# Optimization experiments

Measured on AMD Instinct MI355X. Metric: run time of the kernel, lower is better.

## Reference

```python
import jax, jax.numpy as jnp
import numpy as np

N = 100000   # nodes per node type (individuals and each attribute type)
D = 128      # embedding_size
A = 3        # number of attribute types
P = 50000    # population size
E = 500000   # edges per individual<->attribute edge type
EF = 500000  # family edges


def _seg_mean(msgs, idx, n):
    # PyG 'mean' aggregation: sum / count, empty segments -> 0
    s = jax.ops.segment_sum(msgs, idx, num_segments=n)
    c = jax.ops.segment_sum(jnp.ones((msgs.shape[0],), msgs.dtype), idx, num_segments=n)
    return s / jnp.maximum(c, 1.0)[:, None]


def setup_inputs() -> dict:
    key = jax.random.key(0)
    ks = jax.random.split(key, 20)
    s = 0.05
    return {
        'x_individuals': jax.random.normal(ks[0], (N, D), jnp.float32),
        'x_attributes': jax.random.normal(ks[1], (A, N, D), jnp.float32),
        'positional_features': jax.random.normal(ks[2], (P, A, D), jnp.float32),
        'population': jax.random.permutation(ks[3], N)[:P],  # unique ids (torch indexed assignment with dup ids is UB)
        'edge_index_attr': jax.random.randint(ks[4], (A, 2, E), 0, N),
        'edge_index_family': jax.random.randint(ks[5], (2, EF), 0, N),
        'proj': jax.random.normal(ks[6], (A, D, D), jnp.float32),  # torch.randn(D,D) per attribute
        'agg_W': jax.random.normal(ks[7], (D, 2 * D), jnp.float32) * s,
        'agg_b': jax.random.normal(ks[8], (D,), jnp.float32) * s,
        'W_l1': jax.random.normal(ks[9], (A, D, D), jnp.float32) * s,
        'b_l1': jax.random.normal(ks[10], (A, D), jnp.float32) * s,
        'W_r1': jax.random.normal(ks[11], (A, D, D), jnp.float32) * s,
        'W_l2': jax.random.normal(ks[12], (A, D, D), jnp.float32) * s,
        'b_l2': jax.random.normal(ks[13], (A, D), jnp.float32) * s,
        'W_r2': jax.random.normal(ks[14], (A, D, D), jnp.float32) * s,
        'W_l3': jax.random.normal(ks[15], (D, D), jnp.float32) * s,
        'b_l3': jax.random.normal(ks[16], (D,), jnp.float32) * s,
        'W_r3': jax.random.normal(ks[17], (D, D), jnp.float32) * s,
    }


def reference(x_individuals, x_attributes, positional_features, proj, agg_W, agg_b,
              W_l1, b_l1, W_r1, W_l2, b_l2, W_r2, W_l3, b_l3, W_r3,
              population, edge_index_attr, edge_index_family):
    relu = jax.nn.relu
    src = edge_index_attr[:, 0, :]  # [A,E] individual side
    dst = edge_index_attr[:, 1, :]  # [A,E] attribute side

    # --- stage 0: apply_edges_on_attributes ---
    esf = jnp.einsum('pai,aio->apo', positional_features, proj)          # [A,P,D]
    cat = jnp.concatenate([x_attributes[:, population, :], esf], -1)     # [A,P,2D]
    h = relu(jnp.einsum('api,oi->apo', cat, agg_W) + agg_b)              # Linear(2D->D) + ReLU
    x_att = x_attributes.at[:, population, :].set(h)

    # --- stage 1: SAGEConv individuals -> attributes (source_to_target) ---
    msgs = x_individuals[src]                                            # [A,E,D]
    agg1 = jax.vmap(lambda m, i: _seg_mean(m, i, N))(msgs, dst)          # [A,N,D]
    x_att = (jnp.einsum('ani,aoi->ano', agg1, W_l1) + b_l1[:, None, :]
             + jnp.einsum('ani,aoi->ano', x_att, W_r1))

    # --- stage 2a: apply_edges_on_individuals (per-attribute inverse projection) ---
    M = jnp.linalg.inv(proj) + jnp.eye(D, dtype=proj.dtype)              # [A,D,D]
    upd = relu(jnp.einsum('api,aio->apo', x_att[:, population, :], M))
    x_att = x_att.at[:, population, :].set(upd)

    # --- stage 2b: SAGEConv with flow target_to_source: messages = attribute feats
    # gathered at edge dst, scatter-mean to edge src (individual ids); root term uses x[1]=x_att ---
    msgs2 = jax.vmap(lambda x, i: x[i])(x_att, dst)                      # [A,E,D]
    agg2 = jax.vmap(lambda m, i: _seg_mean(m, i, N))(msgs2, src)         # [A,N,D]
    x_att_out = (jnp.einsum('ani,aoi->ano', agg2, W_l2) + b_l2[:, None, :]
                 + jnp.einsum('ani,aoi->ano', x_att, W_r2))              # stored under attribute keys (PyG HeteroConv dst-keying)

    # --- stage 3: family SAGEConv (target_to_source) on individuals; x_dict['individuals'] was never
    # overwritten by the earlier HeteroConvs (their outputs were keyed by attribute types) ---
    agg3 = _seg_mean(x_individuals[edge_index_family[1]], edge_index_family[0], N)
    x_ind_out = agg3 @ W_l3.T + b_l3 + x_individuals @ W_r3.T

    return x_ind_out, x_att_out
```

## Files before the change

kernel.cpp:

```cpp
#include <hip/hip_runtime.h>
#include <cstddef>

constexpr int Nn  = 100000;
constexpr int Dd  = 128;
constexpr int Aa  = 3;
constexpr int Pp  = 50000;
constexpr int Ee  = 500000;
constexpr int EFf = 500000;
constexpr int REG = Nn + 1;
constexpr int NCSR = 7;
constexpr int T7  = NCSR * REG;
constexpr int RCH = 8;

__global__ void k_invpop(const int* __restrict__ pop, int* __restrict__ invpop){
  int p = blockIdx.x*256 + threadIdx.x;
  if(p < Pp) invpop[pop[p]] = p;
}

__global__ void k_count(const int* __restrict__ eia, const int* __restrict__ fam,
                        int* __restrict__ cnt){
  int tid = blockIdx.x*256 + threadIdx.x;
  if(tid >= NCSR*Ee) return;
  int c = tid / Ee, e = tid - c*Ee;
  const int* key;
  if(c < 3)       key = eia + (c*2+1)*Ee;
  else if(c < 6)  key = eia + ((c-3)*2)*Ee;
  else            key = fam;
  atomicAdd(&cnt[c*REG + key[e]], 1);
}

__global__ void k_fill(const int* __restrict__ eia, const int* __restrict__ fam,
                       int* __restrict__ cursor, int* __restrict__ ebuf){
  int tid = blockIdx.x*256 + threadIdx.x;
  if(tid >= NCSR*Ee) return;
  int c = tid / Ee, e = tid - c*Ee;
  const int *key, *val;
  if(c < 3){      key = eia + (c*2+1)*Ee;      val = eia + (c*2)*Ee; }
  else if(c < 6){ key = eia + ((c-3)*2)*Ee;    val = eia + ((c-3)*2+1)*Ee; }
  else {          key = fam;                   val = fam + EFf; }
  int pos = atomicAdd(&cursor[c*REG + key[e]], 1);
  ebuf[pos] = val[e];
}

__global__ void k_scan_p1(const int* __restrict__ cnt, int* __restrict__ part){
  int b = blockIdx.x;
  int base = b*1024 + threadIdx.x*4;
  int s = 0;
  #pragma unroll
  for(int j=0;j<4;j++){ int idx=base+j; if(idx<T7) s += cnt[idx]; }
  __shared__ int red[256];
  red[threadIdx.x]=s; __syncthreads();
  for(int off=128; off>0; off>>=1){
    if(threadIdx.x<off) red[threadIdx.x]+=red[threadIdx.x+off];
    __syncthreads();
  }
  if(threadIdx.x==0) part[b]=red[0];
}

__global__ void k_scan_p2(int* __restrict__ part, int nchunks){
  __shared__ int buf[256];
  int t = threadIdx.x;
  int carry = 0;
  for(int base=0; base<nchunks; base+=256){
    int i = base+t;
    int v = (i<nchunks)? part[i] : 0;
    buf[t]=v; __syncthreads();
    for(int off=1; off<256; off<<=1){
      int add = (t>=off)? buf[t-off] : 0;
      __syncthreads();
      buf[t]+=add; __syncthreads();
    }
    if(i<nchunks) part[i] = carry + buf[t] - v;
    carry += buf[255];
    __syncthreads();
  }
}

__global__ void k_scan_p3(const int* __restrict__ cnt, const int* __restrict__ part,
                          int* __restrict__ offs, int* __restrict__ cursor){
  int b = blockIdx.x;
  int t = threadIdx.x;
  int idx0 = b*1024 + t*4;
  int v[4]; int s=0;
  #pragma unroll
  for(int j=0;j<4;j++){ int idx=idx0+j; v[j] = (idx<T7)? cnt[idx] : 0; s += v[j]; }
  __shared__ int buf[256];
  buf[t]=s; __syncthreads();
  for(int off=1; off<256; off<<=1){
    int add = (t>=off)? buf[t-off] : 0;
    __syncthreads();
    buf[t]+=add; __syncthreads();
  }
  int excl = buf[t] - s + part[b];
  #pragma unroll
  for(int j=0;j<4;j++){
    int idx=idx0+j;
    if(idx<T7){ offs[idx]=excl; cursor[idx]=excl; }
    excl += v[j];
  }
}

__global__ __launch_bounds__(1024)
void k_gjn(const float* __restrict__ proj, float* __restrict__ Mf32){
  __shared__ float W[128*256];
  __shared__ float pv[128];
  __shared__ float cand_av[2];
  __shared__ float cand_sv[2];
  __shared__ int   cand_ix[2];

  const int a = blockIdx.x;
  const int t = threadIdx.x;
  const int lane = t & 63, wid = t >> 6;
  const float* A = proj + (size_t)a*Dd*Dd;

  for(int idx=t; idx<128*256; idx+=1024){
    int i = idx>>8, c = idx&255;
    float v = (c<128) ? A[(size_t)i*128+c] : ((c-128==i)?1.f:0.f);
    W[idx]=v;
  }
  __syncthreads();

  for(int k=0;k<128;k++){
    if(t < 128){
      float sv = W[t*256+k];
      float av = (t>=k)? fabsf(sv) : -1.f;
      int ix = t;
      #pragma unroll
      for(int off=32; off; off>>=1){
        float oav = __shfl_xor(av, off);
        float osv = __shfl_xor(sv, off);
        int   oix = __shfl_xor(ix, off);
        if(oav > av){ av=oav; sv=osv; ix=oix; }
      }
      if(lane==0){ cand_av[wid]=av; cand_sv[wid]=sv; cand_ix[wid]=ix; }
    }
    __syncthreads();
    const int   pr     = (cand_av[0] >= cand_av[1]) ? cand_ix[0] : cand_ix[1];
    const float pivinv = 1.f / ((cand_av[0] >= cand_av[1]) ? cand_sv[0] : cand_sv[1]);
    if(t < 256){
      int c = t;
      float vk = W[k*256+c];
      float vp = W[pr*256+c];
      W[k*256+c] = ((c==k)?1.f:vp)*pivinv;
      if(pr!=k) W[pr*256+c] = vk;
    }
    __syncthreads();
    if(t < 128) pv[t] = W[t*256+k];
    __syncthreads();
    {
      int c = t&255, g = t>>8;
      float wk = W[k*256+c];
      #pragma unroll
      for(int m=0;m<32;m++){
        int ll = g + m*4;
        if(ll==k) continue;
        float base = (c==k)? 0.f : W[ll*256+c];
        W[ll*256+c] = fmaf(-pv[ll], wk, base);
      }
    }
    __syncthreads();
  }

  for(int idx=t; idx<128*128; idx+=1024){
    int i = idx>>7, c = idx&127;
    W[i*256+c] = A[idx];
  }
  __syncthreads();
  const int i  = t>>3;
  const int j0 = (t&7)*16;
  double acc[16];
  #pragma unroll
  for(int q=0;q<16;q++) acc[q] = (i==j0+q)? 1.0 : 0.0;
  for(int k=0;k<128;k++){
    double aik = (double)W[i*256+k];
    #pragma unroll
    for(int q=0;q<16;q++)
      acc[q] -= aik * (double)W[k*256+128+j0+q];
  }
  __syncthreads();
  #pragma unroll
  for(int q=0;q<16;q++) W[i*256+j0+q] = (float)acc[q];
  __syncthreads();
  #pragma unroll
  for(int q=0;q<16;q++) acc[q] = (double)W[i*256+128+j0+q];
  for(int k=0;k<128;k++){
    double xik = (double)W[i*256+128+k];
    #pragma unroll
    for(int q=0;q<16;q++)
      acc[q] += xik * (double)W[k*256+j0+q];
  }
  float* Mo = Mf32 + (size_t)a*Dd*Dd + (size_t)i*128 + j0;
  #pragma unroll
  for(int q=0;q<16;q++)
    Mo[q] = (float)(acc[q] + ((i==j0+q)? 1.0 : 0.0));
}

template<int MODE>
__launch_bounds__(256)
__global__ void k_gemm(const float* p1, const float* p2, const float* p3,
                       const float* __restrict__ w1p, const float* __restrict__ w2p,
                       const float* __restrict__ biasp,
                       const int* __restrict__ pop, const int* __restrict__ invpop,
                       float* out, int BPA)
{
  constexpr bool NEEDX2 = (MODE==1 || MODE==2 || MODE==4 || MODE==5);
  const int RPA = (MODE==0||MODE==1||MODE==3) ? Pp : Nn;
  const int a    = (MODE==5) ? 0 : (blockIdx.x / BPA);
  const int bidx = (MODE==5) ? blockIdx.x : (blockIdx.x - a*BPA);

  const int t = threadIdx.x;
  const int wave = t >> 6;
  const int lane = t & 63;
  const int o  = wave*32 + (lane>>1);
  const int ih = lane & 1;

  float4 w1v[16]; float4 w2v[16];
  if constexpr(MODE==0 || MODE==3){
    const float* W = w1p + (size_t)a*Dd*Dd;
    #pragma unroll
    for(int jj=0;jj<16;jj++){
      int i0 = ih*64 + jj*4;
      float4 v;
      v.x = W[(size_t)(i0+0)*Dd + o];
      v.y = W[(size_t)(i0+1)*Dd + o];
      v.z = W[(size_t)(i0+2)*Dd + o];
      v.w = W[(size_t)(i0+3)*Dd + o];
      w1v[jj]=v;
    }
  } else if constexpr(MODE==1){
    const float* b1 = w1p + (size_t)o*256 + ih*64;
    const float* b2 = b1 + 128;
    #pragma unroll
    for(int jj=0;jj<16;jj++){
      w1v[jj] = reinterpret_cast<const float4*>(b1)[jj];
      w2v[jj] = reinterpret_cast<const float4*>(b2)[jj];
    }
  } else {
    const size_t ao = (MODE==5)? (size_t)0 : (size_t)a*Dd*Dd;
    const float* W1 = w1p + ao + (size_t)o*Dd + ih*64;
    const float* W2 = w2p + ao + (size_t)o*Dd + ih*64;
    #pragma unroll
    for(int jj=0;jj<16;jj++){
      w1v[jj] = reinterpret_cast<const float4*>(W1)[jj];
      w2v[jj] = reinterpret_cast<const float4*>(W2)[jj];
    }
  }
  float bval = 0.f;
  if constexpr(MODE==1 || MODE==5) bval = biasp[o];
  else if constexpr(MODE==2 || MODE==4) bval = biasp[a*Dd + o];

  __shared__ float xs1[RCH][Dd];
  __shared__ float xs2[NEEDX2 ? RCH : 1][Dd];

  const int chunks = (RPA + RCH - 1)/RCH;
  for(int ch = bidx; ch < chunks; ch += BPA){
    const int r0 = ch*RCH;
    const int nr = min(RCH, RPA - r0);
    {
      int r = t >> 5;
      int q = t & 31;
      if(r < nr){
        int row = r0 + r;
        const float* s1 = nullptr; const float* s2 = nullptr;
        if constexpr(MODE==0){ s1 = p1 + ((size_t)row*Aa + a)*Dd; }
        else if constexpr(MODE==1){
          s1 = p1 + ((size_t)a*Nn + pop[row])*Dd;
          s2 = p3 + ((size_t)a*Pp + row)*Dd;
        }
        else if constexpr(MODE==2){
          s1 = p1 + ((size_t)a*Nn + row)*Dd;
          int ip = invpop[row];
          s2 = (ip>=0) ? (p2 + ((size_t)a*Pp + ip)*Dd)
                       : (p3 + ((size_t)a*Nn + row)*Dd);
        }
        else if constexpr(MODE==3){ s1 = p1 + ((size_t)a*Nn + pop[row])*Dd; }
        else if constexpr(MODE==4){
          s1 = p1 + ((size_t)a*Nn + row)*Dd;
          s2 = p3 + ((size_t)a*Nn + row)*Dd;
        }
        else { s1 = p1 + (size_t)row*Dd; s2 = p3 + (size_t)row*Dd; }
        reinterpret_cast<float4*>(xs1[r])[q] = reinterpret_cast<const float4*>(s1)[q];
        if constexpr(NEEDX2)
          reinterpret_cast<float4*>(xs2[r])[q] = reinterpret_cast<const float4*>(s2)[q];
      }
    }
    __syncthreads();
    for(int r=0;r<nr;r++){
      float acc = 0.f;
      const float4* x1 = reinterpret_cast<const float4*>(xs1[r]) + ih*16;
      #pragma unroll
      for(int jj=0;jj<16;jj++){
        float4 xv = x1[jj]; float4 wv = w1v[jj];
        acc = fmaf(xv.x,wv.x,acc); acc = fmaf(xv.y,wv.y,acc);
        acc = fmaf(xv.z,wv.z,acc); acc = fmaf(xv.w,wv.w,acc);
      }
      if constexpr(NEEDX2){
        const float4* x2 = reinterpret_cast<const float4*>(xs2[r]) + ih*16;
        #pragma unroll
        for(int jj=0;jj<16;jj++){
          float4 xv = x2[jj]; float4 wv = w2v[jj];
          acc = fmaf(xv.x,wv.x,acc); acc = fmaf(xv.y,wv.y,acc);
          acc = fmaf(xv.z,wv.z,acc); acc = fmaf(xv.w,wv.w,acc);
        }
      }
      acc += __shfl_xor(acc, 1, 64);
      if(ih==0){
        float vout = acc;
        if constexpr(MODE==1 || MODE==2 || MODE==4 || MODE==5) vout += bval;
        if constexpr(MODE==1 || MODE==3) vout = fmaxf(vout, 0.f);
        int row = r0 + r;
        size_t orow;
        if constexpr(MODE==0)      orow = (size_t)a*Pp + row;
        else if constexpr(MODE==1) orow = (size_t)a*Pp + row;
        else if constexpr(MODE==2) orow = (size_t)a*Nn + row;
        else if constexpr(MODE==3) orow = (size_t)a*Nn + pop[row];
        else if constexpr(MODE==4) orow = (size_t)a*Nn + row;
        else                       orow = (size_t)row;
        out[orow*Dd + o] = vout;
      }
    }
    __syncthreads();
  }
}

template<int WHICH>
__global__ void k_seg(const float* __restrict__ src, const int* __restrict__ offs,
                      const int* __restrict__ ebuf, float* __restrict__ dst)
{
  const int nw = gridDim.x * 4;
  int gw = (blockIdx.x*256 + threadIdx.x) >> 6;
  const int lane = threadIdx.x & 63;
  const int ROWS = (WHICH==2) ? Nn : Aa*Nn;
  const int cbase = (WHICH==0)?0 : (WHICH==1)?3 : 6;
  for(int row = gw; row < ROWS; row += nw){
    int aa = (WHICH==2)? 0   : row / Nn;
    int n  = (WHICH==2)? row : row - aa*Nn;
    const int* op = offs + (size_t)(cbase+aa)*REG + n;
    int s = op[0], e = op[1];
    float a0=0.f, a1=0.f;
    for(int j=s;j<e;++j){
      int v = ebuf[j];
      const float* rp = src + ((WHICH==1)? ((size_t)aa*Nn+v) : (size_t)v)*Dd;
      a0 += rp[lane]; a1 += rp[lane+64];
    }
    float sc = (e>s)? 1.f/(float)(e-s) : 0.f;
    float* dp = dst + ((WHICH==2)? (size_t)n : ((size_t)aa*Nn+n))*Dd;
    dp[lane]      = a0*sc;
    dp[lane+64]   = a1*sc;
  }
}

extern "C" void kernel_launch(void* const* d_in, const int* in_sizes, int n_in,
                              void* d_out, int out_size, void* d_ws, size_t ws_size,
                              hipStream_t stream)
{
  const float* xind  = (const float*)d_in[0];
  const float* xattr = (const float*)d_in[1];
  const float* posf  = (const float*)d_in[2];
  const int*   pop   = (const int*)  d_in[3];
  const int*   eia   = (const int*)  d_in[4];
  const int*   fam   = (const int*)  d_in[5];
  const float* proj  = (const float*)d_in[6];
  const float* aggW  = (const float*)d_in[7];
  const float* aggb  = (const float*)d_in[8];
  const float* Wl1   = (const float*)d_in[9];
  const float* bl1   = (const float*)d_in[10];
  const float* Wr1   = (const float*)d_in[11];
  const float* Wl2   = (const float*)d_in[12];
  const float* bl2   = (const float*)d_in[13];
  const float* Wr2   = (const float*)d_in[14];
  const float* Wl3   = (const float*)d_in[15];
  const float* bl3   = (const float*)d_in[16];
  const float* Wr3   = (const float*)d_in[17];

  float* outind = (float*)d_out;
  float* outatt = outind + (size_t)Nn*Dd;

  float* h_buf   = (float*)d_ws;
  float* esf_buf = h_buf   + (size_t)Aa*Pp*Dd;
  float* xatt2   = esf_buf + (size_t)Aa*Pp*Dd;
  int*   ebuf    = (int*)(xatt2 + (size_t)Aa*Nn*Dd);
  int*   cnt     = ebuf   + (size_t)NCSR*Ee;
  int*   offs    = cnt    + 700008;
  int*   cursor  = offs   + 700008;
  int*   part    = cursor + 700008;
  int*   invpop  = part   + 1024;
  float* Mf32    = (float*)(invpop + Nn);

  hipMemsetAsync(cnt,    0,    sizeof(int)*700008, stream);
  hipMemsetAsync(invpop, 0xFF, sizeof(int)*Nn,     stream);

  k_invpop<<<(Pp+255)/256, 256, 0, stream>>>(pop, invpop);
  const int egrid = (NCSR*Ee + 255)/256;
  k_count<<<egrid, 256, 0, stream>>>(eia, fam, cnt);
  const int nchunks = (T7 + 1023)/1024;
  k_scan_p1<<<nchunks, 256, 0, stream>>>(cnt, part);
  k_scan_p2<<<1, 256, 0, stream>>>(part, nchunks);
  k_scan_p3<<<nchunks, 256, 0, stream>>>(cnt, part, offs, cursor);
  k_fill<<<egrid, 256, 0, stream>>>(eia, fam, cursor, ebuf);

  k_gjn<<<Aa, 1024, 0, stream>>>(proj, Mf32);

  const int BPA = 240;
  k_gemm<0><<<Aa*BPA, 256, 0, stream>>>(posf, nullptr, nullptr,
                                        proj, nullptr, nullptr,
                                        pop, invpop, esf_buf, BPA);
  k_gemm<1><<<Aa*BPA, 256, 0, stream>>>(xattr, nullptr, esf_buf,
                                        aggW, nullptr, aggb,
                                        pop, invpop, h_buf, BPA);
  k_seg<0><<<1024, 256, 0, stream>>>(xind, offs, ebuf, outatt);
  k_gemm<2><<<Aa*BPA, 256, 0, stream>>>(outatt, h_buf, xattr,
                                        Wl1, Wr1, bl1,
                                        pop, invpop, xatt2, BPA);
  k_gemm<3><<<Aa*BPA, 256, 0, stream>>>(xatt2, nullptr, nullptr,
                                        Mf32, nullptr, nullptr,
                                        pop, invpop, xatt2, BPA);
  k_seg<1><<<1024, 256, 0, stream>>>(xatt2, offs, ebuf, outatt);
  k_gemm<4><<<Aa*BPA, 256, 0, stream>>>(outatt, nullptr, xatt2,
                                        Wl2, Wr2, bl2,
                                        pop, invpop, outatt, BPA);
  k_seg<2><<<1024, 256, 0, stream>>>(xind, offs, ebuf, outind);
  k_gemm<5><<<Aa*BPA, 256, 0, stream>>>(outind, nullptr, xind,
                                        Wl3, Wr3, bl3,
                                        pop, invpop, outind, Aa*BPA);
}
```

Baseline: 3.849 ms.

## Double-buffer row staging in GEMM kernel with register prefetch and larger grids

The row-tile GEMM kernel now loads the next chunk's input rows into registers while the current chunk is computed from shared memory. Shared tiles are double-buffered, which removes the trailing barrier per chunk. Separately, blocks per attribute for the GEMMs rise from 240 to 960 and the segment-mean grids from 1024 to 2048 blocks, to hide more memory latency. The cost is more shared memory and registers per block, plus more blocks each reloading their weight rows.

```diff
diff --git a/kernel.cpp b/kernel.cpp
--- a/kernel.cpp
+++ b/kernel.cpp
@@ -249,45 +249,54 @@
   if constexpr(MODE==1 || MODE==5) bval = biasp[o];
   else if constexpr(MODE==2 || MODE==4) bval = biasp[a*Dd + o];
 
-  __shared__ float xs1[RCH][Dd];
-  __shared__ float xs2[NEEDX2 ? RCH : 1][Dd];
+  __shared__ float xs1[2][RCH][Dd];
+  __shared__ float xs2[2][NEEDX2 ? RCH : 1][Dd];
 
   const int chunks = (RPA + RCH - 1)/RCH;
+  const int r = t >> 5;
+  const int q = t & 31;
+
+  float4 pre1 = {0,0,0,0}, pre2 = {0,0,0,0};
+  auto prefetch = [&](int chp){
+    if(chp >= chunks) return;
+    if(r >= RPA - chp*RCH) return;
+    int row = chp*RCH + r;
+    const float* s1 = nullptr; const float* s2 = nullptr;
+    if constexpr(MODE==0){ s1 = p1 + ((size_t)row*Aa + a)*Dd; }
+    else if constexpr(MODE==1){
+      s1 = p1 + ((size_t)a*Nn + pop[row])*Dd;
+      s2 = p3 + ((size_t)a*Pp + row)*Dd;
+    }
+    else if constexpr(MODE==2){
+      s1 = p1 + ((size_t)a*Nn + row)*Dd;
+      int ip = invpop[row];
+      s2 = (ip>=0) ? (p2 + ((size_t)a*Pp + ip)*Dd)
+                   : (p3 + ((size_t)a*Nn + row)*Dd);
+    }
+    else if constexpr(MODE==3){ s1 = p1 + ((size_t)a*Nn + pop[row])*Dd; }
+    else if constexpr(MODE==4){
+      s1 = p1 + ((size_t)a*Nn + row)*Dd;
+      s2 = p3 + ((size_t)a*Nn + row)*Dd;
+    }
+    else { s1 = p1 + (size_t)row*Dd; s2 = p3 + (size_t)row*Dd; }
+    pre1 = reinterpret_cast<const float4*>(s1)[q];
+    if constexpr(NEEDX2) pre2 = reinterpret_cast<const float4*>(s2)[q];
+  };
+
+  prefetch(bidx);
+  int buf = 0;
   for(int ch = bidx; ch < chunks; ch += BPA){
-    const int r0 = ch*RCH;
-    const int nr = min(RCH, RPA - r0);
-    {
-      int r = t >> 5;
-      int q = t & 31;
-      if(r < nr){
-        int row = r0 + r;
-        const float* s1 = nullptr; const float* s2 = nullptr;
-        if constexpr(MODE==0){ s1 = p1 + ((size_t)row*Aa + a)*Dd; }
-        else if constexpr(MODE==1){
-          s1 = p1 + ((size_t)a*Nn + pop[row])*Dd;
-          s2 = p3 + ((size_t)a*Pp + row)*Dd;
-        }
-        else if constexpr(MODE==2){
-          s1 = p1 + ((size_t)a*Nn + row)*Dd;
-          int ip = invpop[row];
-          s2 = (ip>=0) ? (p2 + ((size_t)a*Pp + ip)*Dd)
-                       : (p3 + ((size_t)a*Nn + row)*Dd);
-        }
-        else if constexpr(MODE==3){ s1 = p1 + ((size_t)a*Nn + pop[row])*Dd; }
-        else if constexpr(MODE==4){
-          s1 = p1 + ((size_t)a*Nn + row)*Dd;
-          s2 = p3 + ((size_t)a*Nn + row)*Dd;
-        }
-        else { s1 = p1 + (size_t)row*Dd; s2 = p3 + (size_t)row*Dd; }
-        reinterpret_cast<float4*>(xs1[r])[q] = reinterpret_cast<const float4*>(s1)[q];
-        if constexpr(NEEDX2)
-          reinterpret_cast<float4*>(xs2[r])[q] = reinterpret_cast<const float4*>(s2)[q];
-      }
-    }
-    __syncthreads();
-    for(int r=0;r<nr;r++){
+    const int nr = min(RCH, RPA - ch*RCH);
+    if(r < nr){
+      reinterpret_cast<float4*>(xs1[buf][r])[q] = pre1;
+      if constexpr(NEEDX2)
+        reinterpret_cast<float4*>(xs2[buf][r])[q] = pre2;
+    }
+    __syncthreads();
+    prefetch(ch + BPA);
+    for(int rr=0; rr<nr; rr++){
       float acc = 0.f;
-      const float4* x1 = reinterpret_cast<const float4*>(xs1[r]) + ih*16;
+      const float4* x1 = reinterpret_cast<const float4*>(xs1[buf][rr]) + ih*16;
       #pragma unroll
       for(int jj=0;jj<16;jj++){
         float4 xv = x1[jj]; float4 wv = w1v[jj];
@@ -295,7 +304,7 @@
         acc = fmaf(xv.z,wv.z,acc); acc = fmaf(xv.w,wv.w,acc);
       }
       if constexpr(NEEDX2){
-        const float4* x2 = reinterpret_cast<const float4*>(xs2[r]) + ih*16;
+        const float4* x2 = reinterpret_cast<const float4*>(xs2[buf][rr]) + ih*16;
         #pragma unroll
         for(int jj=0;jj<16;jj++){
           float4 xv = x2[jj]; float4 wv = w2v[jj];
@@ -308,7 +317,7 @@
         float vout = acc;
         if constexpr(MODE==1 || MODE==2 || MODE==4 || MODE==5) vout += bval;
         if constexpr(MODE==1 || MODE==3) vout = fmaxf(vout, 0.f);
-        int row = r0 + r;
+        int row = ch*RCH + rr;
         size_t orow;
         if constexpr(MODE==0)      orow = (size_t)a*Pp + row;
         else if constexpr(MODE==1) orow = (size_t)a*Pp + row;
@@ -319,7 +328,7 @@
         out[orow*Dd + o] = vout;
       }
     }
-    __syncthreads();
+    buf ^= 1;
   }
 }
 
@@ -401,25 +410,25 @@
 
   k_gjn<<<Aa, 1024, 0, stream>>>(proj, Mf32);
 
-  const int BPA = 240;
+  const int BPA = 960;
   k_gemm<0><<<Aa*BPA, 256, 0, stream>>>(posf, nullptr, nullptr,
                                         proj, nullptr, nullptr,
                                         pop, invpop, esf_buf, BPA);
   k_gemm<1><<<Aa*BPA, 256, 0, stream>>>(xattr, nullptr, esf_buf,
                                         aggW, nullptr, aggb,
                                         pop, invpop, h_buf, BPA);
-  k_seg<0><<<1024, 256, 0, stream>>>(xind, offs, ebuf, outatt);
+  k_seg<0><<<2048, 256, 0, stream>>>(xind, offs, ebuf, outatt);
   k_gemm<2><<<Aa*BPA, 256, 0, stream>>>(outatt, h_buf, xattr,
                                         Wl1, Wr1, bl1,
                                         pop, invpop, xatt2, BPA);
   k_gemm<3><<<Aa*BPA, 256, 0, stream>>>(xatt2, nullptr, nullptr,
                                         Mf32, nullptr, nullptr,
                                         pop, invpop, xatt2, BPA);
-  k_seg<1><<<1024, 256, 0, stream>>>(xatt2, offs, ebuf, outatt);
+  k_seg<1><<<2048, 256, 0, stream>>>(xatt2, offs, ebuf, outatt);
   k_gemm<4><<<Aa*BPA, 256, 0, stream>>>(outatt, nullptr, xatt2,
                                         Wl2, Wr2, bl2,
                                         pop, invpop, outatt, BPA);
-  k_seg<2><<<1024, 256, 0, stream>>>(xind, offs, ebuf, outind);
+  k_seg<2><<<2048, 256, 0, stream>>>(xind, offs, ebuf, outind);
   k_gemm<5><<<Aa*BPA, 256, 0, stream>>>(outind, nullptr, xind,
                                         Wl3, Wr3, bl3,
                                         pop, invpop, outind, Aa*BPA);
```

New measurement: 3.718 ms. -3.4%, faster.
